# Kernel optimization log

Measured on AMD Instinct MI355X. Metric: run time of the kernel, lower is better.

Reference implementation:

```python
import jax, jax.numpy as jnp
import numpy as np

B, T, V, H, L = 32, 128, 50257, 1024, 2


def setup_inputs() -> dict:
    key = jax.random.key(0)
    ks = jax.random.split(key, 8)
    s_in = 0.02   # small init to keep gates unsaturated
    return {
        "tokens": jax.random.randint(ks[0], (B, T), 0, V, dtype=jnp.int32),
        "embedding": jax.random.normal(ks[1], (V, H), jnp.float32) * s_in,
        "W_ih": jax.random.normal(ks[2], (L, 4 * H, H), jnp.float32) * s_in,
        "W_hh": jax.random.normal(ks[3], (L, 4 * H, H), jnp.float32) * s_in,
        "b_ih": jax.random.normal(ks[4], (L, 4 * H), jnp.float32) * s_in,
        "b_hh": jax.random.normal(ks[5], (L, 4 * H), jnp.float32) * s_in,
        "W_out": jax.random.normal(ks[6], (V, H), jnp.float32) * s_in,
        "b_out": jax.random.normal(ks[7], (V,), jnp.float32) * s_in,
        "h0": jnp.zeros((L, B, H), jnp.float32),
        "c0": jnp.zeros((L, B, H), jnp.float32),
    }


def reference(tokens, embedding, W_ih, W_hh, b_ih, b_hh, W_out, b_out, h0, c0):
    # Teacher-forced LSTM LM: embed -> L-layer LSTM (PyTorch gate order i,f,g,o)
    # -> vocab projection -> log-softmax. Dropout is identity (p=0 / eval).
    x = embedding[tokens]                      # [B,T,H]
    xs = jnp.swapaxes(x, 0, 1)                 # [T,B,H] time-major for scan
    n_layers = W_ih.shape[0]

    def step(carry, x_t):
        h, c = carry                           # each [L,B,H]
        inp = x_t
        hs, cs = [], []
        for l in range(n_layers):
            gates = inp @ W_ih[l].T + b_ih[l] + h[l] @ W_hh[l].T + b_hh[l]  # [B,4H]
            i_g, f_g, g_g, o_g = jnp.split(gates, 4, axis=-1)
            i_g = jax.nn.sigmoid(i_g)
            f_g = jax.nn.sigmoid(f_g)
            g_g = jnp.tanh(g_g)
            o_g = jax.nn.sigmoid(o_g)
            c_new = f_g * c[l] + i_g * g_g
            h_new = o_g * jnp.tanh(c_new)
            hs.append(h_new)
            cs.append(c_new)
            inp = h_new
        return (jnp.stack(hs), jnp.stack(cs)), inp

    (hT, cT), outs = jax.lax.scan(step, (h0, c0), xs)   # outs: [T,B,H]
    outs = jnp.swapaxes(outs, 0, 1)                     # [B,T,H]
    logits = outs @ W_out.T + b_out                     # [B,T,V]
    logp = jax.nn.log_softmax(logits, axis=-1)
    return logp, hT, cT
```

## Files before the change

### kernel.cpp

```cpp
#include <hip/hip_runtime.h>
#include <cstdint>
#include <cstddef>

#define DEVI __device__ __forceinline__

typedef __attribute__((ext_vector_type(8))) short short8;
typedef __attribute__((ext_vector_type(4))) float f32x4;
using u16 = unsigned short;

constexpr int BSZ = 32, TSZ = 128, VSZ = 50257, HSZ = 1024;
constexpr int M4 = BSZ * TSZ;
constexpr int FH = 4 * HSZ;
constexpr long long OUT_LOGP = (long long)M4 * VSZ;
constexpr int NWRK = 192;
constexpr int LDSB = 151552;
constexpr int LDBF = 50258;

DEVI u16 f2bf(float f) {
  unsigned u = __float_as_uint(f);
  unsigned r = (u + 0x7fffu + ((u >> 16) & 1u)) >> 16;
  return (u16)r;
}
DEVI float bf2f(u16 u) { return __uint_as_float(((unsigned)u) << 16); }
DEVI float sigm(float x) { return 1.f / (1.f + __expf(-x)); }
DEVI float tanh_fast(float x) { return 1.f - 2.f / (1.f + __expf(2.f * x)); }

DEVI f32x4 mfma16(short8 a, short8 b, f32x4 c) {
  return __builtin_amdgcn_mfma_f32_16x16x32_bf16(a, b, c, 0, 0, 0);
}

DEVI void gld16(const void* g, void* l) {
  auto gp = (const __attribute__((address_space(1))) unsigned int*)g;
  auto lp = (__attribute__((address_space(3))) unsigned int*)l;
  __builtin_amdgcn_global_load_lds(gp, lp, 16, 0, 0);
}

DEVI void cohst2_u16(u16* p0, u16 v0, u16* p1, u16 v1) {
  asm volatile(
      "global_store_short %0, %2, off sc0 sc1\n\t"
      "global_store_short %1, %3, off sc0 sc1\n\t"
      "s_waitcnt vmcnt(0)"
      :: "v"(p0), "v"(p1), "v"((unsigned)v0), "v"((unsigned)v1)
      : "memory");
}
DEVI void cohst1_u16(u16* p0, u16 v0) {
  asm volatile(
      "global_store_short %0, %1, off sc0 sc1\n\t"
      "s_waitcnt vmcnt(0)"
      :: "v"(p0), "v"((unsigned)v0)
      : "memory");
}
DEVI void flagst(unsigned* p, unsigned v) {
  __hip_atomic_store(p, v, __ATOMIC_RELAXED, __HIP_MEMORY_SCOPE_AGENT);
}
DEVI unsigned flagld(const unsigned* p) {
  return __hip_atomic_load(p, __ATOMIC_RELAXED, __HIP_MEMORY_SCOPE_AGENT);
}

DEVI void wait64(const unsigned* f, unsigned g, int l) {
  while (!__all((int)(flagld(f + l) >= g))) __builtin_amdgcn_s_sleep(1);
  __builtin_amdgcn_sched_barrier(0);
}
DEVI void wait128(const unsigned* f, unsigned g, int l) {
  for (;;) {
    unsigned a = flagld(f + l);
    unsigned b = flagld(f + 64 + l);
    if (__all((int)((a >= g) && (b >= g)))) break;
    __builtin_amdgcn_s_sleep(1);
  }
  __builtin_amdgcn_sched_barrier(0);
}

__global__ void prep_misc(const float* __restrict__ bih, const float* __restrict__ bhh,
                          float* __restrict__ bias0, float* __restrict__ rowsum,
                          unsigned* __restrict__ bar) {
  int i = blockIdx.x * 256 + threadIdx.x;
  if (i < FH) { bias0[i] = bih[i] + bhh[i]; rowsum[i] = 0.f; }
  if (i < 1024) bar[i] = 0u;
}

__global__ void prep_h(const float* __restrict__ h0, u16* __restrict__ H0,
                       u16* __restrict__ h1init) {
  int i = blockIdx.x * 256 + threadIdx.x;
  H0[i] = f2bf(h0[i]);
  h1init[i] = f2bf(h0[BSZ * HSZ + i]);
}

__global__ void cvt_bf16(const float* __restrict__ src, u16* __restrict__ dst, int n4) {
  int i = blockIdx.x * blockDim.x + threadIdx.x;
  int stride = gridDim.x * blockDim.x;
  for (; i < n4; i += stride) {
    float4 v = ((const float4*)src)[i];
    ushort4 o; o.x = f2bf(v.x); o.y = f2bf(v.y); o.z = f2bf(v.z); o.w = f2bf(v.w);
    ((ushort4*)dst)[i] = o;
  }
}

__global__ __launch_bounds__(256) void embed_kernel(const int* __restrict__ tok,
                                                    const float* __restrict__ emb,
                                                    u16* __restrict__ X) {
  int m = blockIdx.x;
  int t = m >> 5, b = m & 31;
  int token = tok[b * TSZ + t];
  const float4* src = (const float4*)(emb + (size_t)token * HSZ);
  int i = threadIdx.x;
  float4 v = src[i];
  ushort4 o; o.x = f2bf(v.x); o.y = f2bf(v.y); o.z = f2bf(v.z); o.w = f2bf(v.w);
  *(ushort4*)(X + (size_t)m * HSZ + i * 4) = o;
}

template <int EPI, bool BCVT, int MAP>
__global__ __launch_bounds__(256) void gemm_bt(const u16* __restrict__ A,
                                               const void* __restrict__ Bsrc,
                                               void* __restrict__ Cout,
                                               const float* __restrict__ bias,
                                               float* __restrict__ rowsum,
                                               int nm, int nn, int N, int K, int ldc) {
  __shared__ char smemg[16384];
  u16* As = (u16*)smemg;
  u16* Bs = (u16*)(smemg + 8192);
  float* epi = (float*)smemg;
  const int tid = threadIdx.x;
  int gsz = nm * nn;
  int id = blockIdx.x;
  int bm, bn;
  if constexpr (MAP == 1) {
    const int xcd = id & 7, idx = id >> 3;
    bn = idx >> 2;
    bm = (xcd << 2) + (idx & 3);
  } else {
    int wg = ((gsz & 7) == 0) ? (id % 8) * (gsz >> 3) + (id >> 3) : id;
    bm = wg % nm; bn = wg / nm;
  }
  const int m0 = bm * 128, n0 = bn * 128;
  const int l = tid & 63, wid = tid >> 6;
  const int wm = wid >> 1, wn = wid & 1;

  const int srow = tid >> 2, sq = tid & 3;
  const int arow0 = m0 + srow, arow1 = m0 + 64 + srow;
  int brow0 = n0 + srow;      if (brow0 > N - 1) brow0 = N - 1;
  int brow1 = n0 + 64 + srow; if (brow1 > N - 1) brow1 = N - 1;

  const u16* Bbf = (const u16*)Bsrc;
  const float* Bf32 = (const float*)Bsrc;
  u16* AsW = As + (size_t)(tid >> 6) * 512;
  u16* BsW = Bs + (size_t)(tid >> 6) * 512;

  f32x4 acc[4][4];
  f32x4 z = {0.f, 0.f, 0.f, 0.f};
#pragma unroll
  for (int a = 0; a < 4; ++a)
#pragma unroll
    for (int b = 0; b < 4; ++b) acc[a][b] = z;

  for (int k0 = 0; k0 < K; k0 += 32) {
    gld16(A + (size_t)arow0 * K + k0 + sq * 8, AsW);
    gld16(A + (size_t)arow1 * K + k0 + sq * 8, AsW + 2048);
    if (!BCVT) {
      gld16(Bbf + (size_t)brow0 * K + k0 + sq * 8, BsW);
      gld16(Bbf + (size_t)brow1 * K + k0 + sq * 8, BsW + 2048);
    } else {
      const float* s0 = Bf32 + (size_t)brow0 * K + k0 + sq * 8;
      const float* s1 = Bf32 + (size_t)brow1 * K + k0 + sq * 8;
      float4 x0 = *(const float4*)s0, y0 = *(const float4*)(s0 + 4);
      float4 x1 = *(const float4*)s1, y1 = *(const float4*)(s1 + 4);
      short8 v0, v1;
      v0[0]=(short)f2bf(x0.x); v0[1]=(short)f2bf(x0.y); v0[2]=(short)f2bf(x0.z); v0[3]=(short)f2bf(x0.w);
      v0[4]=(short)f2bf(y0.x); v0[5]=(short)f2bf(y0.y); v0[6]=(short)f2bf(y0.z); v0[7]=(short)f2bf(y0.w);
      v1[0]=(short)f2bf(x1.x); v1[1]=(short)f2bf(x1.y); v1[2]=(short)f2bf(x1.z); v1[3]=(short)f2bf(x1.w);
      v1[4]=(short)f2bf(y1.x); v1[5]=(short)f2bf(y1.y); v1[6]=(short)f2bf(y1.z); v1[7]=(short)f2bf(y1.w);
      *(short8*)&Bs[(size_t)tid * 8] = v0;
      *(short8*)&Bs[(size_t)tid * 8 + 2048] = v1;
    }
    __syncthreads();
    short8 af[4], bfr[4];
#pragma unroll
    for (int x = 0; x < 4; ++x) {
      int ar = wm * 64 + x * 16 + (l & 15);
      af[x] = *(const short8*)&As[ar * 32 + ((l >> 4) << 3)];
      int br = wn * 64 + x * 16 + (l & 15);
      bfr[x] = *(const short8*)&Bs[br * 32 + ((l >> 4) << 3)];
    }
#pragma unroll
    for (int mf = 0; mf < 4; ++mf)
#pragma unroll
      for (int nf = 0; nf < 4; ++nf)
        acc[mf][nf] = mfma16(af[mf], bfr[nf], acc[mf][nf]);
    __syncthreads();
  }

  if constexpr (EPI == 2) {
    u16* C = (u16*)Cout;
#pragma unroll
    for (int mf = 0; mf < 4; ++mf) {
      int rbase = m0 + wm * 64 + mf * 16 + ((l >> 4) << 2);
      float bvr[4];
#pragma unroll
      for (int j = 0; j < 4; ++j) bvr[j] = bias[rbase + j];
#pragma unroll
      for (int nf = 0; nf < 4; ++nf) {
        int cg = n0 + wn * 64 + nf * 16 + (l & 15);
#pragma unroll
        for (int j = 0; j < 4; ++j)
          C[(size_t)(rbase + j) * ldc + cg] = f2bf(acc[mf][nf][j] + bvr[j]);
      }
    }
  } else if constexpr (EPI == 3) {
    u16* C = (u16*)Cout;
    float* ep = epi + wid * 1024;
    const int lq4 = l >> 4, l15e = l & 15;
    float bv[4];
#pragma unroll
    for (int nf = 0; nf < 4; ++nf) {
      int cg = n0 + wn * 64 + nf * 16 + l15e;
      bv[nf] = (cg < N) ? bias[cg] : 0.f;
    }
    const int r8 = l >> 3, c8 = l & 7;
    const int colb8 = n0 + wn * 64 + c8 * 8;
#pragma unroll
    for (int mf = 0; mf < 4; ++mf) {
#pragma unroll
      for (int nf = 0; nf < 4; ++nf)
#pragma unroll
        for (int j = 0; j < 4; ++j)
          ep[(lq4 * 4 + j) * 64 + nf * 16 + l15e] = acc[mf][nf][j] + bv[nf];
      asm volatile("s_waitcnt lgkmcnt(0)" ::: "memory");
      __builtin_amdgcn_sched_barrier(0);
#pragma unroll
      for (int pass = 0; pass < 2; ++pass) {
        const int rr = pass * 8 + r8;
        f32x4 v0 = *(const f32x4*)&ep[rr * 64 + c8 * 8];
        f32x4 v1 = *(const f32x4*)&ep[rr * 64 + c8 * 8 + 4];
        const int row = m0 + wm * 64 + mf * 16 + rr;
        float e = 0.f;
        if (colb8 + 7 < N) {
          short8 o;
          o[0]=(short)f2bf(v0[0]); o[1]=(short)f2bf(v0[1]);
          o[2]=(short)f2bf(v0[2]); o[3]=(short)f2bf(v0[3]);
          o[4]=(short)f2bf(v1[0]); o[5]=(short)f2bf(v1[1]);
          o[6]=(short)f2bf(v1[2]); o[7]=(short)f2bf(v1[3]);
          *(short8*)&C[(size_t)row * ldc + colb8] = o;
          e = __expf(v0[0]) + __expf(v0[1]) + __expf(v0[2]) + __expf(v0[3]) +
              __expf(v1[0]) + __expf(v1[1]) + __expf(v1[2]) + __expf(v1[3]);
        } else {
#pragma unroll
          for (int kk = 0; kk < 8; ++kk) {
            float fv = (kk < 4) ? v0[kk] : v1[kk - 4];
            if (colb8 + kk < N) {
              C[(size_t)row * ldc + colb8 + kk] = f2bf(fv);
              e += __expf(fv);
            }
          }
        }
        e += __shfl_xor(e, 1, 8); e += __shfl_xor(e, 2, 8); e += __shfl_xor(e, 4, 8);
        if (c8 == 0) atomicAdd(&rowsum[row], e);
      }
      asm volatile("s_waitcnt lgkmcnt(0)" ::: "memory");
      __builtin_amdgcn_sched_barrier(0);
    }
  } else {
    float* C = (float*)Cout;
    float* ep = epi + wid * 1024;
    const int lq4 = l >> 4, l15e = l & 15;
    float bv[4];
#pragma unroll
    for (int nf = 0; nf < 4; ++nf) {
      int cg = n0 + wn * 64 + nf * 16 + l15e;
      bv[nf] = (cg < N) ? bias[cg] : 0.f;
    }
    const int colbase = n0 + wn * 64 + l15e * 4;
#pragma unroll
    for (int mf = 0; mf < 4; ++mf) {
#pragma unroll
      for (int nf = 0; nf < 4; ++nf)
#pragma unroll
        for (int j = 0; j < 4; ++j)
          ep[(lq4 * 4 + j) * 64 + nf * 16 + l15e] = acc[mf][nf][j] + bv[nf];
      asm volatile("s_waitcnt lgkmcnt(0)" ::: "memory");
      __builtin_amdgcn_sched_barrier(0);
#pragma unroll
      for (int pass = 0; pass < 4; ++pass) {
        const int rr = pass * 4 + lq4;
        f32x4 v = *(const f32x4*)&ep[rr * 64 + l15e * 4];
        const int row = m0 + wm * 64 + mf * 16 + rr;
        float e = 0.f;
        if (colbase + 3 < N) {
          *(f32x4*)&C[(size_t)row * ldc + colbase] = v;
          e = __expf(v[0]) + __expf(v[1]) + __expf(v[2]) + __expf(v[3]);
        } else {
#pragma unroll
          for (int kk = 0; kk < 4; ++kk)
            if (colbase + kk < N) {
              C[(size_t)row * ldc + colbase + kk] = v[kk];
              e += __expf(v[kk]);
            }
        }
        e += __shfl_xor(e, 1, 16); e += __shfl_xor(e, 2, 16);
        e += __shfl_xor(e, 4, 16); e += __shfl_xor(e, 8, 16);
        if (l15e == 0) atomicAdd(&rowsum[row], e);
      }
      asm volatile("s_waitcnt lgkmcnt(0)" ::: "memory");
      __builtin_amdgcn_sched_barrier(0);
    }
  }
}

struct LstmArgs {
  const u16* G0T;
  const float* Wih;
  const float* Whh;
  const float* bih, *bhh, *c0;
  u16* H0;
  u16* H1;
  const u16* h1init;
  float* out_hc;
  unsigned* bar;
};

DEVI void stage_row_q(const float* src, char* row, int sw, int q) {
  for (int kk = 0; kk < 256; kk += 8) {
    float4 x = *(const float4*)(src + kk);
    float4 y = *(const float4*)(src + kk + 4);
    short8 v;
    v[0]=(short)f2bf(x.x); v[1]=(short)f2bf(x.y); v[2]=(short)f2bf(x.z); v[3]=(short)f2bf(x.w);
    v[4]=(short)f2bf(y.x); v[5]=(short)f2bf(y.y); v[6]=(short)f2bf(y.z); v[7]=(short)f2bf(y.w);
    const int kbyte = (q * 256 + kk) * 2;
    *(short8*)(row + (kbyte ^ sw)) = v;
  }
}

DEVI short8 ldsB(const char* lds, int r, int kbyte) {
  return *(const short8*)(lds + (size_t)r * 2048 + (kbyte ^ ((r & 7) << 4)));
}

DEVI void part_wr(float* part, int wblk, int wv, int R, int lq, f32x4 v) {
  *(f32x4*)&part[wv * wblk + R * 20 + lq * 4] = v;
}
DEVI float part_rd(const float* part, int wblk, int wv, int R, int c) {
  return part[wv * wblk + R * 20 + c];
}

__global__ __launch_bounds__(256, 1) void lstm_coop(LstmArgs A) {
  extern __shared__ char smem[];
  const int wg = blockIdx.x, tid = threadIdx.x;
  const int wv = tid >> 6, l = tid & 63;
  const int l15 = l & 15, lq = l >> 4;
  const int bh = wv >> 1, kh = wv & 1;

  if (wg < 64) {
    char* WL = smem;
    float* part = (float*)(smem + 131072);
    const int j0 = wg << 4;
    {
      const int R = tid >> 2, q = tid & 3;
      const int grow = ((R >> 4) << 10) + j0 + (R & 15);
      stage_row_q(A.Whh + (size_t)grow * HSZ + q * 256, WL + (size_t)R * 2048,
                  (R & 7) << 4, q);
    }
    const int uu = tid & 15, bb = tid >> 4;
    float cst[2];
    cst[0] = A.c0[(size_t)bb * HSZ + j0 + uu];
    cst[1] = A.c0[(size_t)(bb + 16) * HSZ + j0 + uu];
    __syncthreads();
    unsigned* myflag = A.bar + wg;

    for (int t = 0; t < TSZ; ++t) {
      float g0v[4][2];
      {
        const int col = t * 32;
#pragma unroll
        for (int g4 = 0; g4 < 4; ++g4) {
          const u16* gp = A.G0T + (size_t)((g4 << 10) + j0 + uu) * M4 + col;
          g0v[g4][0] = bf2f(gp[bb]);
          g0v[g4][1] = bf2f(gp[bb + 16]);
        }
      }
      if (t > 0) wait64(A.bar, (unsigned)t, l);
      const u16* hprev = A.H0 + (size_t)t * (BSZ * HSZ);
      const u16* hb = hprev + (size_t)(bh * 16 + l15) * HSZ + (kh << 9) + (lq << 3);
      short8 a[16];
#pragma unroll
      for (int k = 0; k < 16; ++k) a[k] = *(const short8*)(hb + k * 32);
      f32x4 acc[4];
      { f32x4 z = {0.f,0.f,0.f,0.f}; acc[0]=z; acc[1]=z; acc[2]=z; acc[3]=z; }
#pragma unroll
      for (int k = 0; k < 16; ++k) {
        const int kbyte = (((kh << 4) + k) << 6) + (lq << 4);
#pragma unroll
        for (int tr = 0; tr < 4; ++tr)
          acc[tr] = mfma16(a[k], ldsB(WL, (tr << 4) + l15, kbyte), acc[tr]);
      }
#pragma unroll
      for (int tr = 0; tr < 4; ++tr)
        part_wr(part, 1280, wv, (tr << 4) + l15, lq, acc[tr]);
      __syncthreads();
      const bool last = (t == TSZ - 1);
      u16* hnext = A.H0 + (size_t)(t + 1) * (BSZ * HSZ);
      u16 hv[2];
#pragma unroll
      for (int pp = 0; pp < 2; ++pp) {
        const int b = bb + (pp << 4);
        float gi = g0v[0][pp], gf = g0v[1][pp], gg = g0v[2][pp], go = g0v[3][pp];
#pragma unroll
        for (int kh2 = 0; kh2 < 2; ++kh2) {
          const int w2 = (pp << 1) | kh2;
          gi += part_rd(part, 1280, w2, uu, bb);
          gf += part_rd(part, 1280, w2, 16 + uu, bb);
          gg += part_rd(part, 1280, w2, 32 + uu, bb);
          go += part_rd(part, 1280, w2, 48 + uu, bb);
        }
        float i_ = sigm(gi), f_ = sigm(gf), g_ = tanh_fast(gg), o_ = sigm(go);
        float c_ = f_ * cst[pp] + i_ * g_;
        cst[pp] = c_;
        float h_ = o_ * tanh_fast(c_);
        hv[pp] = f2bf(h_);
        if (last) {
          A.out_hc[(size_t)b * HSZ + j0 + uu] = h_;
          A.out_hc[2 * BSZ * HSZ + (size_t)b * HSZ + j0 + uu] = c_;
        }
      }
      cohst2_u16(hnext + (size_t)bb * HSZ + j0 + uu, hv[0],
                 hnext + (size_t)(bb + 16) * HSZ + j0 + uu, hv[1]);
      __syncthreads();
      if (tid == 0) flagst(myflag, (unsigned)(t + 1));
    }
  } else {
    char* WxL = smem;
    char* WhL = smem + 65536;
    float* part = (float*)(smem + 131072);
    float* biasL = (float*)(smem + 141312);
    const int lw = wg - 64;
    const int j1 = lw << 3;
    {
      const int rr = tid >> 2, q = tid & 3;
      const int r = rr & 31;
      const int grow = FH + ((r >> 3) << 10) + j1 + (r & 7);
      const float* base = (rr >= 32) ? A.Whh : A.Wih;
      char* dst = ((rr >= 32) ? WhL : WxL) + (size_t)r * 2048;
      stage_row_q(base + (size_t)grow * HSZ + q * 256, dst, (r & 7) << 4, q);
    }
    if (tid < 32) {
      const int grow = FH + ((tid >> 3) << 10) + j1 + (tid & 7);
      biasL[tid] = A.bih[grow] + A.bhh[grow];
    }
    const int uu = tid & 7, b1 = tid >> 3;
    float cst = A.c0[BSZ * HSZ + (size_t)b1 * HSZ + j1 + uu];
    __syncthreads();
    unsigned* myflag = A.bar + 64 + lw;

    for (int t = 0; t < TSZ; ++t) {
      wait64(A.bar, (unsigned)(t + 1), l);
      const u16* x1 = A.H0 + (size_t)(t + 1) * (BSZ * HSZ);
      const u16* xb = x1 + (size_t)(bh * 16 + l15) * HSZ + (kh << 9) + (lq << 3);
      short8 ax[16];
#pragma unroll
      for (int k = 0; k < 16; ++k) ax[k] = *(const short8*)(xb + k * 32);
      f32x4 acc[2];
      { f32x4 z = {0.f,0.f,0.f,0.f}; acc[0]=z; acc[1]=z; }
#pragma unroll
      for (int k = 0; k < 16; ++k) {
        const int kbyte = (((kh << 4) + k) << 6) + (lq << 4);
        acc[0] = mfma16(ax[k], ldsB(WxL, l15, kbyte), acc[0]);
        acc[1] = mfma16(ax[k], ldsB(WxL, 16 + l15, kbyte), acc[1]);
      }
      if (t > 0) wait128(A.bar + 64, (unsigned)t, l);
      const u16* hp = (t == 0) ? A.h1init : A.H1 + (size_t)(t - 1) * HSZ;
      const size_t hstr = (t == 0) ? (size_t)HSZ : (size_t)TSZ * HSZ;
      const u16* hbp = hp + (size_t)(bh * 16 + l15) * hstr + (kh << 9) + (lq << 3);
      short8 ah[16];
#pragma unroll
      for (int k = 0; k < 16; ++k) ah[k] = *(const short8*)(hbp + k * 32);
#pragma unroll
      for (int k = 0; k < 16; ++k) {
        const int kbyte = (((kh << 4) + k) << 6) + (lq << 4);
        acc[0] = mfma16(ah[k], ldsB(WhL, l15, kbyte), acc[0]);
        acc[1] = mfma16(ah[k], ldsB(WhL, 16 + l15, kbyte), acc[1]);
      }
#pragma unroll
      for (int tr = 0; tr < 2; ++tr)
        part_wr(part, 640, wv, (tr << 4) + l15, lq, acc[tr]);
      __syncthreads();
      const bool last = (t == TSZ - 1);
      {
        const int c = b1 & 15, ph = b1 >> 4;
        float gi = biasL[uu], gf = biasL[8 + uu], gg = biasL[16 + uu], go = biasL[24 + uu];
#pragma unroll
        for (int kh2 = 0; kh2 < 2; ++kh2) {
          const int w2 = (ph << 1) | kh2;
          gi += part_rd(part, 640, w2, uu, c);
          gf += part_rd(part, 640, w2, 8 + uu, c);
          gg += part_rd(part, 640, w2, 16 + uu, c);
          go += part_rd(part, 640, w2, 24 + uu, c);
        }
        float i_ = sigm(gi), f_ = sigm(gf), g_ = tanh_fast(gg), o_ = sigm(go);
        float c_ = f_ * cst + i_ * g_;
        cst = c_;
        float h_ = o_ * tanh_fast(c_);
        cohst1_u16(A.H1 + (size_t)b1 * (TSZ * HSZ) + (size_t)t * HSZ + j1 + uu, f2bf(h_));
        if (last) {
          A.out_hc[BSZ * HSZ + (size_t)b1 * HSZ + j1 + uu] = h_;
          A.out_hc[3 * BSZ * HSZ + (size_t)b1 * HSZ + j1 + uu] = c_;
        }
      }
      __syncthreads();
      if (tid == 0) flagst(myflag, (unsigned)(t + 1));
    }
  }
}

__global__ void lse_kernel(float* __restrict__ rowsum, int n) {
  int i = blockIdx.x * 256 + threadIdx.x;
  if (i < n) rowsum[i] = logf(rowsum[i]);
}

__global__ __launch_bounds__(256) void lsm_finish(float* __restrict__ C,
                                                  const float* __restrict__ lse, int Vd) {
  int row = blockIdx.y;
  size_t start = (size_t)row * (size_t)Vd;
  float s = lse[row];
  int i = blockIdx.x * 256 + threadIdx.x;
  int col = i * 4;
  if (col + 3 < Vd) {
    f32x4* p = (f32x4*)(C + start + col);
    f32x4 v = *p;
    v[0] -= s; v[1] -= s; v[2] -= s; v[3] -= s;
    *p = v;
  } else {
    for (int j = col; j < Vd; ++j) C[start + j] -= s;
  }
}

__global__ __launch_bounds__(256) void lsm_finish_bf(const u16* __restrict__ L,
                                                     float* __restrict__ out,
                                                     const float* __restrict__ lse,
                                                     int Vd, int ldl) {
  int row = blockIdx.y;
  float s = lse[row];
  int col = blockIdx.x * 2048 + threadIdx.x * 8;
  const u16* lp = L + (size_t)row * ldl;
  float* op = out + (size_t)row * Vd;
  if (col + 7 < Vd) {
    short8 v = *(const short8*)(lp + col);
    f32x4 a, b;
    a[0] = bf2f((u16)v[0]) - s; a[1] = bf2f((u16)v[1]) - s;
    a[2] = bf2f((u16)v[2]) - s; a[3] = bf2f((u16)v[3]) - s;
    b[0] = bf2f((u16)v[4]) - s; b[1] = bf2f((u16)v[5]) - s;
    b[2] = bf2f((u16)v[6]) - s; b[3] = bf2f((u16)v[7]) - s;
    *(f32x4*)(op + col) = a;
    *(f32x4*)(op + col + 4) = b;
  } else {
    for (int j = col; j < Vd; ++j) op[j] = bf2f(lp[j]) - s;
  }
}

extern "C" void kernel_launch(void* const* d_in, const int* in_sizes, int n_in,
                              void* d_out, int out_size, void* d_ws, size_t ws_size,
                              hipStream_t stream) {
  const int* tokens = (const int*)d_in[0];
  const float* emb = (const float*)d_in[1];
  const float* Wih = (const float*)d_in[2];
  const float* Whh = (const float*)d_in[3];
  const float* bih = (const float*)d_in[4];
  const float* bhh = (const float*)d_in[5];
  const float* Wout = (const float*)d_in[6];
  const float* bout = (const float*)d_in[7];
  const float* h0 = (const float*)d_in[8];
  const float* c0 = (const float*)d_in[9];
  float* out = (float*)d_out;

  char* w = (char*)d_ws;
  size_t o = 0;
  u16* Xbf = (u16*)(w + o);    o += (size_t)M4 * HSZ * 2;
  u16* Wih0bf = (u16*)(w + o); o += (size_t)FH * HSZ * 2;
  u16* G0T = (u16*)(w + o);    o += (size_t)FH * M4 * 2;
  u16* H0 = (u16*)(w + o);     o += (size_t)(TSZ + 1) * BSZ * HSZ * 2;
  u16* H1 = (u16*)(w + o);     o += (size_t)BSZ * TSZ * HSZ * 2;
  u16* h1init = (u16*)(w + o); o += (size_t)BSZ * HSZ * 2;
  float* bias0 = (float*)(w + o);  o += FH * 4;
  float* rowsum = (float*)(w + o); o += M4 * 4;
  unsigned* bar = (unsigned*)(w + o); o += 4096;
  u16* Woutbf = (u16*)(w + o);
  size_t need_full = o + (size_t)VSZ * HSZ * 2;
  u16* Lbf = (u16*)(w + need_full);
  size_t need_lbf = need_full + (size_t)M4 * LDBF * 2;
  const bool bcvt = (ws_size < need_full);
  const bool bf16c = (ws_size >= need_lbf);

  prep_misc<<<16, 256, 0, stream>>>(bih, bhh, bias0, rowsum, bar);
  prep_h<<<128, 256, 0, stream>>>(h0, H0, h1init);
  cvt_bf16<<<2048, 256, 0, stream>>>(Wih, Wih0bf, FH * HSZ / 4);
  if (!bcvt)
    cvt_bf16<<<4096, 256, 0, stream>>>(Wout, Woutbf, (int)((size_t)VSZ * HSZ / 4));
  embed_kernel<<<M4, 256, 0, stream>>>(tokens, emb, Xbf);
  gemm_bt<2, false, 0><<<32 * 32, 256, 0, stream>>>(Wih0bf, Xbf, G0T, bias0, nullptr,
                                                    32, 32, M4, HSZ, M4);

  LstmArgs la{G0T, Wih, Whh, bih, bhh, c0, H0, H1, h1init,
              out + (size_t)OUT_LOGP, bar};
  void* kargs[] = {&la};
  hipFuncSetAttribute((const void*)lstm_coop, hipFuncAttributeMaxDynamicSharedMemorySize, LDSB);
  hipLaunchCooperativeKernel((const void*)lstm_coop, dim3(NWRK), dim3(256), kargs, LDSB, stream);

  const int nn = (VSZ + 127) / 128;
  if (bf16c) {
    gemm_bt<3, false, 1><<<32 * nn, 256, 0, stream>>>(H1, Woutbf, Lbf, bout, rowsum,
                                                      32, nn, VSZ, HSZ, LDBF);
  } else if (!bcvt) {
    gemm_bt<1, false, 1><<<32 * nn, 256, 0, stream>>>(H1, Woutbf, out, bout, rowsum,
                                                      32, nn, VSZ, HSZ, VSZ);
  } else {
    gemm_bt<1, true, 1><<<32 * nn, 256, 0, stream>>>(H1, Wout, out, bout, rowsum,
                                                     32, nn, VSZ, HSZ, VSZ);
  }

  lse_kernel<<<16, 256, 0, stream>>>(rowsum, M4);
  if (bf16c)
    lsm_finish_bf<<<dim3(25, M4), 256, 0, stream>>>(Lbf, out, rowsum, VSZ, LDBF);
  else
    lsm_finish<<<dim3((VSZ + 1023) / 1024, M4), 256, 0, stream>>>(out, rowsum, VSZ);
}
```

Measured before the change: 1.837 ms.

## Interleave gate rows so MFMA output holds all four gates per lane

```diff
diff --git a/kernel.cpp b/kernel.cpp
--- a/kernel.cpp
+++ b/kernel.cpp
@@ -13,7 +13,7 @@
 constexpr int FH = 4 * HSZ;
 constexpr long long OUT_LOGP = (long long)M4 * VSZ;
 constexpr int NWRK = 192;
-constexpr int LDSB = 151552;
+constexpr int LDSB = 131072;
 constexpr int LDBF = 50258;
 
 DEVI u16 f2bf(float f) {
@@ -333,173 +333,168 @@
   return *(const short8*)(lds + (size_t)r * 2048 + (kbyte ^ ((r & 7) << 4)));
 }
 
-DEVI void part_wr(float* part, int wblk, int wv, int R, int lq, f32x4 v) {
-  *(f32x4*)&part[wv * wblk + R * 20 + lq * 4] = v;
-}
-DEVI float part_rd(const float* part, int wblk, int wv, int R, int c) {
-  return part[wv * wblk + R * 20 + c];
-}
-
 __global__ __launch_bounds__(256, 1) void lstm_coop(LstmArgs A) {
   extern __shared__ char smem[];
   const int wg = blockIdx.x, tid = threadIdx.x;
   const int wv = tid >> 6, l = tid & 63;
   const int l15 = l & 15, lq = l >> 4;
-  const int bh = wv >> 1, kh = wv & 1;
+  const int bh = wv >> 1;
 
   if (wg < 64) {
     char* WL = smem;
-    float* part = (float*)(smem + 131072);
+    const int uo = wv & 1;
     const int j0 = wg << 4;
     {
       const int R = tid >> 2, q = tid & 3;
-      const int grow = ((R >> 4) << 10) + j0 + (R & 15);
+      const int tt = R >> 4, r = R & 15;
+      const int ul = ((tt >> 1) << 3) + ((tt & 1) << 2) + (r >> 2);
+      const int grow = ((r & 3) << 10) + j0 + ul;
       stage_row_q(A.Whh + (size_t)grow * HSZ + q * 256, WL + (size_t)R * 2048,
                   (R & 7) << 4, q);
     }
-    const int uu = tid & 15, bb = tid >> 4;
+    const int b = (bh << 4) + l15;
+    const int u0 = j0 + (uo << 3) + lq;
+    const int u1 = u0 + 4;
     float cst[2];
-    cst[0] = A.c0[(size_t)bb * HSZ + j0 + uu];
-    cst[1] = A.c0[(size_t)(bb + 16) * HSZ + j0 + uu];
+    cst[0] = A.c0[(size_t)b * HSZ + u0];
+    cst[1] = A.c0[(size_t)b * HSZ + u1];
     __syncthreads();
     unsigned* myflag = A.bar + wg;
 
     for (int t = 0; t < TSZ; ++t) {
-      float g0v[4][2];
+      f32x4 acc0, acc1;
       {
-        const int col = t * 32;
-#pragma unroll
-        for (int g4 = 0; g4 < 4; ++g4) {
-          const u16* gp = A.G0T + (size_t)((g4 << 10) + j0 + uu) * M4 + col;
-          g0v[g4][0] = bf2f(gp[bb]);
-          g0v[g4][1] = bf2f(gp[bb + 16]);
+        const int col = t * 32 + b;
+#pragma unroll
+        for (int j = 0; j < 4; ++j) {
+          acc0[j] = bf2f(A.G0T[(size_t)((j << 10) + u0) * M4 + col]);
+          acc1[j] = bf2f(A.G0T[(size_t)((j << 10) + u1) * M4 + col]);
         }
       }
       if (t > 0) wait64(A.bar, (unsigned)t, l);
-      const u16* hprev = A.H0 + (size_t)t * (BSZ * HSZ);
-      const u16* hb = hprev + (size_t)(bh * 16 + l15) * HSZ + (kh << 9) + (lq << 3);
-      short8 a[16];
-#pragma unroll
-      for (int k = 0; k < 16; ++k) a[k] = *(const short8*)(hb + k * 32);
-      f32x4 acc[4];
-      { f32x4 z = {0.f,0.f,0.f,0.f}; acc[0]=z; acc[1]=z; acc[2]=z; acc[3]=z; }
-#pragma unroll
-      for (int k = 0; k < 16; ++k) {
-        const int kbyte = (((kh << 4) + k) << 6) + (lq << 4);
-#pragma unroll
-        for (int tr = 0; tr < 4; ++tr)
-          acc[tr] = mfma16(a[k], ldsB(WL, (tr << 4) + l15, kbyte), acc[tr]);
-      }
-#pragma unroll
-      for (int tr = 0; tr < 4; ++tr)
-        part_wr(part, 1280, wv, (tr << 4) + l15, lq, acc[tr]);
-      __syncthreads();
+      const u16* hrow = A.H0 + (size_t)t * (BSZ * HSZ) + (size_t)((bh << 4) + l15) * HSZ + (lq << 3);
+      const int R0 = (uo << 5), R1 = R0 + 16;
+#pragma unroll
+      for (int half = 0; half < 2; ++half) {
+        short8 hf[16];
+#pragma unroll
+        for (int k = 0; k < 16; ++k)
+          hf[k] = *(const short8*)(hrow + (half * 16 + k) * 32);
+#pragma unroll
+        for (int k = 0; k < 16; ++k) {
+          const int kbyte = ((half * 16 + k) << 6) + (lq << 4);
+          acc0 = mfma16(ldsB(WL, R0 + l15, kbyte), hf[k], acc0);
+          acc1 = mfma16(ldsB(WL, R1 + l15, kbyte), hf[k], acc1);
+        }
+      }
       const bool last = (t == TSZ - 1);
       u16* hnext = A.H0 + (size_t)(t + 1) * (BSZ * HSZ);
       u16 hv[2];
-#pragma unroll
-      for (int pp = 0; pp < 2; ++pp) {
-        const int b = bb + (pp << 4);
-        float gi = g0v[0][pp], gf = g0v[1][pp], gg = g0v[2][pp], go = g0v[3][pp];
-#pragma unroll
-        for (int kh2 = 0; kh2 < 2; ++kh2) {
-          const int w2 = (pp << 1) | kh2;
-          gi += part_rd(part, 1280, w2, uu, bb);
-          gf += part_rd(part, 1280, w2, 16 + uu, bb);
-          gg += part_rd(part, 1280, w2, 32 + uu, bb);
-          go += part_rd(part, 1280, w2, 48 + uu, bb);
-        }
-        float i_ = sigm(gi), f_ = sigm(gf), g_ = tanh_fast(gg), o_ = sigm(go);
-        float c_ = f_ * cst[pp] + i_ * g_;
-        cst[pp] = c_;
+      {
+        float i_ = sigm(acc0[0]), f_ = sigm(acc0[1]);
+        float g_ = tanh_fast(acc0[2]), o_ = sigm(acc0[3]);
+        float c_ = f_ * cst[0] + i_ * g_;
+        cst[0] = c_;
         float h_ = o_ * tanh_fast(c_);
-        hv[pp] = f2bf(h_);
+        hv[0] = f2bf(h_);
         if (last) {
-          A.out_hc[(size_t)b * HSZ + j0 + uu] = h_;
-          A.out_hc[2 * BSZ * HSZ + (size_t)b * HSZ + j0 + uu] = c_;
-        }
-      }
-      cohst2_u16(hnext + (size_t)bb * HSZ + j0 + uu, hv[0],
-                 hnext + (size_t)(bb + 16) * HSZ + j0 + uu, hv[1]);
+          A.out_hc[(size_t)b * HSZ + u0] = h_;
+          A.out_hc[2 * BSZ * HSZ + (size_t)b * HSZ + u0] = c_;
+        }
+      }
+      {
+        float i_ = sigm(acc1[0]), f_ = sigm(acc1[1]);
+        float g_ = tanh_fast(acc1[2]), o_ = sigm(acc1[3]);
+        float c_ = f_ * cst[1] + i_ * g_;
+        cst[1] = c_;
+        float h_ = o_ * tanh_fast(c_);
+        hv[1] = f2bf(h_);
+        if (last) {
+          A.out_hc[(size_t)b * HSZ + u1] = h_;
+          A.out_hc[2 * BSZ * HSZ + (size_t)b * HSZ + u1] = c_;
+        }
+      }
+      cohst2_u16(hnext + (size_t)b * HSZ + u0, hv[0],
+                 hnext + (size_t)b * HSZ + u1, hv[1]);
       __syncthreads();
       if (tid == 0) flagst(myflag, (unsigned)(t + 1));
     }
   } else {
     char* WxL = smem;
     char* WhL = smem + 65536;
-    float* part = (float*)(smem + 131072);
-    float* biasL = (float*)(smem + 141312);
+    const int uh = wv & 1;
     const int lw = wg - 64;
     const int j1 = lw << 3;
     {
-      const int rr = tid >> 2, q = tid & 3;
-      const int r = rr & 31;
-      const int grow = FH + ((r >> 3) << 10) + j1 + (r & 7);
-      const float* base = (rr >= 32) ? A.Whh : A.Wih;
-      char* dst = ((rr >= 32) ? WhL : WxL) + (size_t)r * 2048;
+      const int R = tid >> 2, q = tid & 3;
+      const int r = R & 15, tt = (R >> 4) & 1;
+      const int ul = (tt << 2) + (r >> 2);
+      const int grow = FH + ((r & 3) << 10) + j1 + ul;
+      const float* base = (R >= 32) ? A.Whh : A.Wih;
+      char* dst = ((R >= 32) ? WhL : WxL) + (size_t)(((R >> 4) & 1) * 16 + r) * 2048;
       stage_row_q(base + (size_t)grow * HSZ + q * 256, dst, (r & 7) << 4, q);
     }
-    if (tid < 32) {
-      const int grow = FH + ((tid >> 3) << 10) + j1 + (tid & 7);
-      biasL[tid] = A.bih[grow] + A.bhh[grow];
-    }
-    const int uu = tid & 7, b1 = tid >> 3;
-    float cst = A.c0[BSZ * HSZ + (size_t)b1 * HSZ + j1 + uu];
+    const int b = (bh << 4) + l15;
+    const int u = j1 + (uh << 2) + lq;
+    float bv[4];
+#pragma unroll
+    for (int j = 0; j < 4; ++j) {
+      const int grow = FH + (j << 10) + u;
+      bv[j] = A.bih[grow] + A.bhh[grow];
+    }
+    float cst = A.c0[BSZ * HSZ + (size_t)b * HSZ + u];
     __syncthreads();
     unsigned* myflag = A.bar + 64 + lw;
+    const int Rb = uh << 4;
 
     for (int t = 0; t < TSZ; ++t) {
       wait64(A.bar, (unsigned)(t + 1), l);
-      const u16* x1 = A.H0 + (size_t)(t + 1) * (BSZ * HSZ);
-      const u16* xb = x1 + (size_t)(bh * 16 + l15) * HSZ + (kh << 9) + (lq << 3);
-      short8 ax[16];
-#pragma unroll
-      for (int k = 0; k < 16; ++k) ax[k] = *(const short8*)(xb + k * 32);
-      f32x4 acc[2];
-      { f32x4 z = {0.f,0.f,0.f,0.f}; acc[0]=z; acc[1]=z; }
-#pragma unroll
-      for (int k = 0; k < 16; ++k) {
-        const int kbyte = (((kh << 4) + k) << 6) + (lq << 4);
-        acc[0] = mfma16(ax[k], ldsB(WxL, l15, kbyte), acc[0]);
-        acc[1] = mfma16(ax[k], ldsB(WxL, 16 + l15, kbyte), acc[1]);
+      f32x4 acc = {bv[0], bv[1], bv[2], bv[3]};
+      {
+        const u16* xrow = A.H0 + (size_t)(t + 1) * (BSZ * HSZ) +
+                          (size_t)((bh << 4) + l15) * HSZ + (lq << 3);
+#pragma unroll
+        for (int half = 0; half < 2; ++half) {
+          short8 xf[16];
+#pragma unroll
+          for (int k = 0; k < 16; ++k)
+            xf[k] = *(const short8*)(xrow + (half * 16 + k) * 32);
+#pragma unroll
+          for (int k = 0; k < 16; ++k) {
+            const int kbyte = ((half * 16 + k) << 6) + (lq << 4);
+            acc = mfma16(ldsB(WxL, Rb + l15, kbyte), xf[k], acc);
+          }
+        }
       }
       if (t > 0) wait128(A.bar + 64, (unsigned)t, l);
-      const u16* hp = (t == 0) ? A.h1init : A.H1 + (size_t)(t - 1) * HSZ;
-      const size_t hstr = (t == 0) ? (size_t)HSZ : (size_t)TSZ * HSZ;
-      const u16* hbp = hp + (size_t)(bh * 16 + l15) * hstr + (kh << 9) + (lq << 3);
-      short8 ah[16];
-#pragma unroll
-      for (int k = 0; k < 16; ++k) ah[k] = *(const short8*)(hbp + k * 32);
-#pragma unroll
-      for (int k = 0; k < 16; ++k) {
-        const int kbyte = (((kh << 4) + k) << 6) + (lq << 4);
-        acc[0] = mfma16(ah[k], ldsB(WhL, l15, kbyte), acc[0]);
-        acc[1] = mfma16(ah[k], ldsB(WhL, 16 + l15, kbyte), acc[1]);
-      }
-#pragma unroll
-      for (int tr = 0; tr < 2; ++tr)
-        part_wr(part, 640, wv, (tr << 4) + l15, lq, acc[tr]);
-      __syncthreads();
+      {
+        const u16* hp = (t == 0) ? A.h1init : A.H1 + (size_t)(t - 1) * HSZ;
+        const size_t hstr = (t == 0) ? (size_t)HSZ : (size_t)TSZ * HSZ;
+        const u16* hrow = hp + (size_t)((bh << 4) + l15) * hstr + (lq << 3);
+#pragma unroll
+        for (int half = 0; half < 2; ++half) {
+          short8 hf[16];
+#pragma unroll
+          for (int k = 0; k < 16; ++k)
+            hf[k] = *(const short8*)(hrow + (half * 16 + k) * 32);
+#pragma unroll
+          for (int k = 0; k < 16; ++k) {
+            const int kbyte = ((half * 16 + k) << 6) + (lq << 4);
+            acc = mfma16(ldsB(WhL, Rb + l15, kbyte), hf[k], acc);
+          }
+        }
+      }
       const bool last = (t == TSZ - 1);
       {
-        const int c = b1 & 15, ph = b1 >> 4;
-        float gi = biasL[uu], gf = biasL[8 + uu], gg = biasL[16 + uu], go = biasL[24 + uu];
-#pragma unroll
-        for (int kh2 = 0; kh2 < 2; ++kh2) {
-          const int w2 = (ph << 1) | kh2;
-          gi += part_rd(part, 640, w2, uu, c);
-          gf += part_rd(part, 640, w2, 8 + uu, c);
-          gg += part_rd(part, 640, w2, 16 + uu, c);
-          go += part_rd(part, 640, w2, 24 + uu, c);
-        }
-        float i_ = sigm(gi), f_ = sigm(gf), g_ = tanh_fast(gg), o_ = sigm(go);
+        float i_ = sigm(acc[0]), f_ = sigm(acc[1]);
+        float g_ = tanh_fast(acc[2]), o_ = sigm(acc[3]);
         float c_ = f_ * cst + i_ * g_;
         cst = c_;
         float h_ = o_ * tanh_fast(c_);
-        cohst1_u16(A.H1 + (size_t)b1 * (TSZ * HSZ) + (size_t)t * HSZ + j1 + uu, f2bf(h_));
+        cohst1_u16(A.H1 + (size_t)b * (TSZ * HSZ) + (size_t)t * HSZ + u, f2bf(h_));
         if (last) {
-          A.out_hc[BSZ * HSZ + (size_t)b1 * HSZ + j1 + uu] = h_;
-          A.out_hc[3 * BSZ * HSZ + (size_t)b1 * HSZ + j1 + uu] = c_;
+          A.out_hc[BSZ * HSZ + (size_t)b * HSZ + u] = h_;
+          A.out_hc[3 * BSZ * HSZ + (size_t)b * HSZ + u] = c_;
         }
       }
       __syncthreads();
```

Result: slower. 2.184 ms (+18.9%).
